# Performance work log

Hardware: AMD Instinct MI355X
Metric: run time of the kernel (lower is better)

The kernel has to match this reference:

```python
import jax, jax.numpy as jnp
import numpy as np

K = 20          # knn
EPS = 1e-5      # InstanceNorm2d eps
NEG_SLOPE = 0.2 # LeakyReLU slope


def setup_inputs() -> dict:
    key = jax.random.key(0)
    k1, k2 = jax.random.split(key)
    B, C, N = 4, 64, 4096
    out_dim, in_dim = 64, 2 * C
    batch = jax.random.normal(k1, (B, C, N), dtype=jnp.float32)
    # Conv2d(in_dim, out_dim, kernel_size=1, bias=False) weight, squeezed to [out,in]
    W = jax.random.normal(k2, (out_dim, in_dim), dtype=jnp.float32) * (1.0 / np.sqrt(in_dim))
    return {"batch": batch, "W": W}


def reference(batch, W):
    x = batch  # [B, C, N]
    # --- KNNGraph: pairwise squared distances + top-k nearest ---
    xx = jnp.sum(x * x, axis=1)                      # [B, N]
    inner = jnp.einsum('bcn,bcm->bnm', x, x)         # [B, N, N]
    neg_dist = -(xx[:, :, None] - 2.0 * inner + xx[:, None, :])  # [B, N, N]
    _, idx = jax.lax.top_k(neg_dist, K)              # [B, N, K] nearest neighbors
    # --- edge feature gather: concat(x_j - x_i, x_i) -> [B, 2C, N, K] ---
    nbr = jax.vmap(lambda xb, ib: xb[:, ib])(x, idx) # [B, C, N, K]
    center = x[:, :, :, None]                        # [B, C, N, 1]
    edge = jnp.concatenate([nbr - center, jnp.broadcast_to(center, nbr.shape)], axis=1)
    # --- 1x1 Conv2d (shared MLP, no bias) ---
    y = jnp.einsum('oc,bcnk->bonk', W, edge)         # [B, out, N, K]
    # --- InstanceNorm2d (no affine, biased var over spatial dims) ---
    mean = jnp.mean(y, axis=(2, 3), keepdims=True)
    var = jnp.var(y, axis=(2, 3), keepdims=True)
    y = (y - mean) * jax.lax.rsqrt(var + EPS)
    # --- LeakyReLU(0.2) ---
    y = jnp.where(y >= 0, y, NEG_SLOPE * y)
    # --- MaxPool over neighbor dim ---
    return jnp.max(y, axis=3)                        # [B, out, N]
```

## Files before the change

### kernel.cpp

```cpp
#include <hip/hip_runtime.h>
#include <hip/hip_bf16.h>
#include <cstdint>
#include <cstddef>

#define BB 4
#define NN 4096
#define NROW (BB*NN)
#define CAP3 128
#define ZSTAR 2.17f
#define SLACK 0.30

typedef float v2f   __attribute__((ext_vector_type(2)));
typedef float f32x16 __attribute__((ext_vector_type(16)));
typedef short s16x8 __attribute__((ext_vector_type(8)));
typedef _Float16 f16x8 __attribute__((ext_vector_type(8)));

__device__ __forceinline__ v2f pkfma(v2f a, v2f b, v2f c) {
  return __builtin_elementwise_fma(a, b, c);
}

__global__ __launch_bounds__(256) void k1_prep(
    const float* __restrict__ x, const float* __restrict__ W,
    float* __restrict__ xT, unsigned short* __restrict__ xh,
    float* __restrict__ xxf, double* __restrict__ xxd, float* __restrict__ Trow,
    float* __restrict__ uT, float* __restrict__ vT)
{
  __shared__ float xc[64][65];
  __shared__ float xr[64][68];
  __shared__ float w1[64][65];
  __shared__ float wd[64][65];
  int t = threadIdx.x;
  int b  = blockIdx.x >> 6;
  int n0 = (blockIdx.x & 63) * 64;

  for (int i = t; i < 4096; i += 256) {
    int o = i >> 6, c = i & 63;
    float a = W[o*128 + c];
    w1[o][c] = a;
    wd[o][c] = W[o*128 + 64 + c] - a;
  }
  for (int i = t; i < 4096; i += 256) {
    int c = i >> 6, n = i & 63;
    xc[c][n] = x[((size_t)b*64 + c)*4096 + n0 + n];
  }
  __syncthreads();

  for (int i = t; i < 4096; i += 256) {
    int n = i >> 6, c = i & 63;
    float v = xc[c][n];
    xr[n][c] = v;
    size_t pi = ((size_t)b*4096 + n0 + n)*64 + c;
    xT[pi] = v;
    xh[pi] = __builtin_bit_cast(unsigned short, (_Float16)v);
  }
  if (t < 64) {
    int n = t;
    float s0=0,s1=0,s2=0,s3=0; double sd=0.0;
    for (int c = 0; c < 64; c += 4) {
      float a0=xc[c][n],a1=xc[c+1][n],a2=xc[c+2][n],a3=xc[c+3][n];
      s0=fmaf(a0,a0,s0); s1=fmaf(a1,a1,s1); s2=fmaf(a2,a2,s2); s3=fmaf(a3,a3,s3);
      sd += (double)a0*a0 + (double)a1*a1 + (double)a2*a2 + (double)a3*a3;
    }
    float xxv = (s0+s1)+(s2+s3);
    size_t ri = (size_t)b*4096 + n0 + n;
    xxf[ri] = xxv;
    xxd[ri] = sd;
    Trow[ri] = fmaf(-ZSTAR, sqrtf(fmaf(4.0f, xxv, 128.0f)), 64.0f);
  }
  v2f w1r[32], wdr[32];
  int o = t & 63;
  #pragma unroll
  for (int j = 0; j < 32; ++j) {
    w1r[j].x = w1[o][2*j]; w1r[j].y = w1[o][2*j+1];
    wdr[j].x = wd[o][2*j]; wdr[j].y = wd[o][2*j+1];
  }
  __syncthreads();

  for (int i = t; i < 4096; i += 256) {
    int n = i >> 6;
    v2f au; au.x=0.f; au.y=0.f;
    v2f av; av.x=0.f; av.y=0.f;
    #pragma unroll
    for (int cb = 0; cb < 16; ++cb) {
      float4 xv = *(const float4*)&xr[n][cb*4];
      v2f p0; p0.x = xv.x; p0.y = xv.y;
      v2f p1; p1.x = xv.z; p1.y = xv.w;
      au = pkfma(w1r[2*cb],   p0, au);
      au = pkfma(w1r[2*cb+1], p1, au);
      av = pkfma(wdr[2*cb],   p0, av);
      av = pkfma(wdr[2*cb+1], p1, av);
    }
    size_t idx = ((size_t)b*4096 + n0 + n)*64 + o;
    uT[idx] = au.x + au.y;
    vT[idx] = av.x + av.y;
  }
}

__global__ __launch_bounds__(256) void k2_screen(
    const unsigned short* __restrict__ xh, const float* __restrict__ xxf,
    const float* __restrict__ Trow, unsigned* __restrict__ bitmap)
{
  int t  = threadIdx.x;
  int nb = blockIdx.x >> 4;
  int ms = blockIdx.x & 15;
  int row0 = nb * 256;
  int b = row0 >> 12;
  int mbase = ms * 256;
  const unsigned short* xhB = xh + ((size_t)b*4096)*64;

  int wv = t >> 6, lane = t & 63;
  int lr = lane & 31, oct = lane >> 5;

  s16x8 ah[2][4];
  #pragma unroll
  for (int nt = 0; nt < 2; ++nt)
    #pragma unroll
    for (int ks = 0; ks < 4; ++ks)
      ah[nt][ks] = *(const s16x8*)(xh +
        ((size_t)(row0 + wv*64 + nt*32 + lr))*64 + ks*16 + oct*8);

  float Ta[16], Tb[16];
  #pragma unroll
  for (int i = 0; i < 16; ++i) {
    int bi = (i & 3) + 8*(i >> 2);
    Ta[i] = Trow[row0 + wv*64 + bi + 4*oct];
    Tb[i] = Trow[row0 + wv*64 + 32 + bi + 4*oct];
  }

  unsigned mreg[8];
  #pragma unroll
  for (int mt = 0; mt < 8; ++mt) {
    int m0 = mbase + mt*32;
    float xxm = xxf[b*4096 + m0 + lr];
    s16x8 bh[4];
    #pragma unroll
    for (int ks = 0; ks < 4; ++ks)
      bh[ks] = *(const s16x8*)(xhB + (size_t)(m0 + lr)*64 + ks*16 + oct*8);

    f32x16 a0, a1;
    #pragma unroll
    for (int i = 0; i < 16; ++i) { a0[i] = 0.f; a1[i] = 0.f; }
    #pragma unroll
    for (int ks = 0; ks < 4; ++ks) {
      f16x8 AH0 = __builtin_bit_cast(f16x8, ah[0][ks]);
      f16x8 AH1 = __builtin_bit_cast(f16x8, ah[1][ks]);
      f16x8 BH  = __builtin_bit_cast(f16x8, bh[ks]);
      a0 = __builtin_amdgcn_mfma_f32_32x32x16_f16(AH0, BH, a0, 0, 0, 0);
      a1 = __builtin_amdgcn_mfma_f32_32x32x16_f16(AH1, BH, a1, 0, 0, 0);
    }

    unsigned mymask = 0u;
    #pragma unroll
    for (int i = 0; i < 16; ++i) {
      const int base_i = (i & 3) + 8*(i >> 2);
      {
        float w = fmaf(-2.0f, a0[i], xxm);
        unsigned long long mk = __ballot(w < Ta[i]);
        mymask = (lane == base_i)     ? (unsigned)mk         : mymask;
        mymask = (lane == base_i + 4) ? (unsigned)(mk >> 32) : mymask;
      }
      {
        float w = fmaf(-2.0f, a1[i], xxm);
        unsigned long long mk = __ballot(w < Tb[i]);
        mymask = (lane == 32 + base_i) ? (unsigned)mk         : mymask;
        mymask = (lane == 36 + base_i) ? (unsigned)(mk >> 32) : mymask;
      }
    }
    mreg[mt] = mymask;
  }

  size_t grow = (size_t)(row0 + wv*64 + lane);
  uint4 lo4; lo4.x = mreg[0]; lo4.y = mreg[1]; lo4.z = mreg[2]; lo4.w = mreg[3];
  uint4 hi4; hi4.x = mreg[4]; hi4.y = mreg[5]; hi4.z = mreg[6]; hi4.w = mreg[7];
  *(uint4*)&bitmap[grow*128 + ms*8]     = lo4;
  *(uint4*)&bitmap[grow*128 + ms*8 + 4] = hi4;
}

__global__ __launch_bounds__(256) void k3_select(
    const float* __restrict__ xT, const double* __restrict__ xxd,
    const float* __restrict__ Trow, const unsigned* __restrict__ bitmap,
    const float* __restrict__ uT, const float* __restrict__ vT,
    float* __restrict__ stage, double* __restrict__ pS1, double* __restrict__ pS2,
    unsigned* __restrict__ slowcnt, unsigned* __restrict__ slowlist)
{
  __shared__ unsigned short candm[4][CAP3];
  int wv = threadIdx.x >> 6, lane = threadIdx.x & 63;
  int row = blockIdx.x * 4 + wv;
  int b = row >> 12;

  double s1t = 0.0, s2t = 0.0;
  double xxn = xxd[row];

  uint2 wds = *(const uint2*)&bitmap[(size_t)row*128 + lane*2];
  int myc = __popc(wds.x) + __popc(wds.y);
  int inc = myc;
  #pragma unroll
  for (int d = 1; d < 64; d <<= 1) {
    int v = __shfl_up(inc, d);
    if (lane >= d) inc += v;
  }
  int total = __shfl(inc, 63);
  int off = inc - myc;
  bool slow = (total < 20) || (total > CAP3);

  if (!slow) {
    unsigned w = wds.x; int mb = lane*64;
    while (w) { int j = __ffs(w) - 1; w &= w - 1;
                candm[wv][off++] = (unsigned short)(mb + j); }
    w = wds.y; mb = lane*64 + 32;
    while (w) { int j = __ffs(w) - 1; w &= w - 1;
                candm[wv][off++] = (unsigned short)(mb + j); }
  }
  __builtin_amdgcn_wave_barrier();

  if (!slow) {
    const float* pn = xT + (size_t)row*64;
    int nr = (total + 63) >> 6;
    unsigned long long L = ~0ull;
    for (int r = 0; r < nr; ++r) {
      int ci = r*64 + lane;
      unsigned long long S = ~0ull;
      if (ci < total) {
        int m = (int)candm[wv][ci];
        const float* pm = xT + ((size_t)b*4096 + m)*64;
        double acc0 = 0.0, acc1 = 0.0;
        #pragma unroll
        for (int c5 = 0; c5 < 64; c5 += 4) {
          float4 A = *(const float4*)(pn + c5);
          float4 B = *(const float4*)(pm + c5);
          acc0 = fma((double)A.x, (double)B.x, acc0);
          acc1 = fma((double)A.y, (double)B.y, acc1);
          acc0 = fma((double)A.z, (double)B.z, acc0);
          acc1 = fma((double)A.w, (double)B.w, acc1);
        }
        double d = xxn + xxd[(size_t)b*4096 + m] - 2.0*(acc0 + acc1);
        d = fmax(d, 0.0);
        S = (((unsigned long long)__double_as_longlong(d)) & ~0xFFFull)
          | (unsigned long long)m;
      }
      #pragma unroll
      for (int kk = 2; kk <= 64; kk <<= 1) {
        #pragma unroll
        for (int j = kk >> 1; j > 0; j >>= 1) {
          unsigned long long o = __shfl_xor(S, j);
          bool up    = ((lane & kk) == 0);
          bool lower = ((lane & j) == 0);
          unsigned long long mn = (S < o) ? S : o;
          unsigned long long mx = (S < o) ? o : S;
          S = (lower == up) ? mn : mx;
        }
      }
      if (r == 0) {
        L = S;
      } else {
        unsigned long long Sr = __shfl(S, 63 - lane);
        unsigned long long lo = (L < Sr) ? L : Sr;
        #pragma unroll
        for (int j = 32; j > 0; j >>= 1) {
          unsigned long long o = __shfl_xor(lo, j);
          unsigned long long mn = (lo < o) ? lo : o;
          unsigned long long mx = (lo < o) ? o : lo;
          lo = ((lane & j) == 0) ? mn : mx;
        }
        L = lo;
      }
    }
    unsigned long long k19 = __shfl(L, 19);
    double d20 = __longlong_as_double((long long)(k19 & ~0xFFFull));
    float Tr = Trow[row];
    if (!(d20 - xxn < (double)Tr - SLACK)) {
      slow = true;
    } else {
      int mlow = (int)(L & 0xFFFull);
      const float* ub = uT + (size_t)b*4096*64;
      float mx = -3.4e38f, s1 = 0.f, s2 = 0.f;
      #pragma unroll
      for (int k = 0; k < 20; ++k) {
        int m = __shfl(mlow, k);
        float g = ub[(size_t)m*64 + lane];
        mx = fmaxf(mx, g); s1 += g; s2 = fmaf(g, g, s2);
      }
      size_t ro = (size_t)row*64 + lane;
      float v = vT[ro];
      stage[ro] = mx + v;
      double dv = (double)v;
      s1t = (double)s1 + 20.0*dv;
      s2t = (double)s2 + 2.0*dv*(double)s1 + 20.0*dv*dv;
    }
  }
  if (slow && lane == 0) {
    unsigned i = atomicAdd(slowcnt, 1u); slowlist[i] = row;
  }
  pS1[(size_t)row*64 + lane] = s1t;
  pS2[(size_t)row*64 + lane] = s2t;
}

__global__ __launch_bounds__(256) void k3b_slow(
    const float* __restrict__ xT, const double* __restrict__ xxd,
    const unsigned* __restrict__ slowcnt, const unsigned* __restrict__ slowlist,
    const float* __restrict__ uT, const float* __restrict__ vT,
    float* __restrict__ stage, double* __restrict__ k3bS1, double* __restrict__ k3bS2)
{
  __shared__ unsigned long long keyl[4096];
  __shared__ unsigned long long red[4];
  __shared__ unsigned t20[20];
  unsigned nslow = *slowcnt;
  int t = threadIdx.x;
  for (unsigned ii = blockIdx.x; ii < nslow; ii += gridDim.x) {
    int row = (int)slowlist[ii];
    int b = row >> 12, n = row & 4095;
    const float* pn = xT + ((size_t)b*4096 + n)*64;
    double xxn = xxd[(size_t)b*4096 + n];
    for (int m = t; m < 4096; m += 256) {
      const float* pm = xT + ((size_t)b*4096 + m)*64;
      double acc = 0.0;
      #pragma unroll 4
      for (int c = 0; c < 64; c += 4) {
        float4 a  = *(const float4*)(pn + c);
        float4 bf = *(const float4*)(pm + c);
        acc = fma((double)a.x, (double)bf.x, acc);
        acc = fma((double)a.y, (double)bf.y, acc);
        acc = fma((double)a.z, (double)bf.z, acc);
        acc = fma((double)a.w, (double)bf.w, acc);
      }
      double d = fmax(xxn + xxd[(size_t)b*4096 + m] - 2.0*acc, 0.0);
      keyl[m] = (((unsigned long long)__double_as_longlong(d)) & ~0xFFFull)
              | (unsigned long long)m;
    }
    __syncthreads();
    for (int k = 0; k < 20; ++k) {
      unsigned long long mn = ~0ull;
      #pragma unroll
      for (int s = 0; s < 16; ++s) {
        unsigned long long v = keyl[t + s*256];
        mn = (v < mn) ? v : mn;
      }
      for (int off = 32; off > 0; off >>= 1) {
        unsigned long long o = __shfl_down(mn, off);
        mn = (o < mn) ? o : mn;
      }
      if ((t & 63) == 0) red[t >> 6] = mn;
      __syncthreads();
      if (t == 0) {
        unsigned long long w0 = red[0];
        for (int q = 1; q < 4; ++q) w0 = (red[q] < w0) ? red[q] : w0;
        t20[k] = (unsigned)(w0 & 0xFFFull);
        keyl[w0 & 0xFFFull] = ~0ull;
      }
      __syncthreads();
    }
    if (t < 64) {
      const float* ub = uT + (size_t)b*4096*64;
      float mx = -3.4e38f, s1 = 0.f, s2 = 0.f;
      #pragma unroll
      for (int k = 0; k < 20; ++k) {
        unsigned m = t20[k];
        float g = ub[(size_t)m*64 + t];
        mx = fmaxf(mx, g); s1 += g; s2 = fmaf(g, g, s2);
      }
      size_t ro = ((size_t)b*4096 + n)*64 + t;
      float v = vT[ro];
      stage[ro] = mx + v;
      double dv = (double)v;
      __hip_atomic_fetch_add(&k3bS1[b*64 + t], (double)s1 + 20.0*dv,
                             __ATOMIC_RELAXED, __HIP_MEMORY_SCOPE_AGENT);
      __hip_atomic_fetch_add(&k3bS2[b*64 + t], (double)s2 + 2.0*dv*(double)s1 + 20.0*dv*dv,
                             __ATOMIC_RELAXED, __HIP_MEMORY_SCOPE_AGENT);
    }
    __syncthreads();
  }
}

__global__ __launch_bounds__(256) void k4a1_reduce(
    const double* __restrict__ pS1, const double* __restrict__ pS2,
    double* __restrict__ part1, double* __restrict__ part2)
{
  __shared__ double r1[4][64], r2[4][64];
  int blk = blockIdx.x;
  int t = threadIdx.x, wv = t >> 6, o = t & 63;
  size_t rbase = (size_t)blk*64 + wv*16;
  double s1 = 0.0, s2 = 0.0;
  for (int j = 0; j < 16; ++j) {
    s1 += pS1[(rbase + j)*64 + o];
    s2 += pS2[(rbase + j)*64 + o];
  }
  r1[wv][o] = s1; r2[wv][o] = s2;
  __syncthreads();
  if (wv == 0) {
    part1[(size_t)blk*64 + o] = r1[0][o]+r1[1][o]+r1[2][o]+r1[3][o];
    part2[(size_t)blk*64 + o] = r2[0][o]+r2[1][o]+r2[2][o]+r2[3][o];
  }
}

__global__ __launch_bounds__(256) void k4a2_params(
    const double* __restrict__ part1, const double* __restrict__ part2,
    const double* __restrict__ k3bS1, const double* __restrict__ k3bS2,
    float2* __restrict__ params)
{
  __shared__ double r1[4][64], r2[4][64];
  int b = blockIdx.x;
  int t = threadIdx.x, wv = t >> 6, o = t & 63;
  double s1 = 0.0, s2 = 0.0;
  for (int j = wv*16; j < wv*16 + 16; ++j) {
    s1 += part1[((size_t)b*64 + j)*64 + o];
    s2 += part2[((size_t)b*64 + j)*64 + o];
  }
  r1[wv][o] = s1; r2[wv][o] = s2;
  __syncthreads();
  if (wv == 0) {
    double S1 = k3bS1[b*64 + o] + r1[0][o]+r1[1][o]+r1[2][o]+r1[3][o];
    double S2 = k3bS2[b*64 + o] + r2[0][o]+r2[1][o]+r2[2][o]+r2[3][o];
    double inv = 1.0 / (4096.0 * 20.0);
    double mean = S1 * inv;
    double var  = S2 * inv - mean * mean;
    float2 pr; pr.x = (float)mean; pr.y = (float)rsqrt(var + 1e-5);
    params[b*64 + o] = pr;
  }
}

__global__ __launch_bounds__(256) void k4b_final(
    const float* __restrict__ stage, const float2* __restrict__ params,
    float* __restrict__ out)
{
  __shared__ float tile[64][65];
  int blk = blockIdx.x;
  int b = blk >> 6, n0 = (blk & 63) * 64;
  int t = threadIdx.x;
  int o = t & 63;
  float2 pr = params[b*64 + o];
  for (int i = t; i < 4096; i += 256) {
    int nn = i >> 6;
    float y = (stage[((size_t)b*4096 + n0 + nn)*64 + o] - pr.x) * pr.y;
    tile[nn][o] = (y >= 0.f) ? y : 0.2f * y;
  }
  __syncthreads();
  for (int i = t; i < 4096; i += 256) {
    int oo = i >> 6, nn = i & 63;
    out[((size_t)(b*64 + oo))*4096 + n0 + nn] = tile[nn][oo];
  }
}

extern "C" void kernel_launch(void* const* d_in, const int* in_sizes, int n_in,
                              void* d_out, int out_size, void* d_ws, size_t ws_size,
                              hipStream_t stream)
{
  (void)in_sizes; (void)n_in; (void)out_size; (void)ws_size;
  const float* x = (const float*)d_in[0];
  const float* W = (const float*)d_in[1];
  float* out = (float*)d_out;

  char* ws = (char*)d_ws;
  size_t off = 0;
  auto alloc = [&](size_t bytes) {
    char* p = ws + off;
    off = (off + bytes + 255) & ~(size_t)255;
    return p;
  };
  float*          uT       = (float*)         alloc((size_t)NROW*64*4);
  float*          vT       = (float*)         alloc((size_t)NROW*64*4);
  float*          xT       = (float*)         alloc((size_t)NROW*64*4);
  float*          stage    = (float*)         alloc((size_t)NROW*64*4);
  unsigned short* xh       = (unsigned short*)alloc((size_t)NROW*64*2);
  float*          xxf      = (float*)         alloc((size_t)NROW*4);
  double*         xxd      = (double*)        alloc((size_t)NROW*8);
  float*          Trow     = (float*)         alloc((size_t)NROW*4);
  double*         pS1      = (double*)        alloc((size_t)NROW*64*8);
  double*         pS2      = (double*)        alloc((size_t)NROW*64*8);
  double*         part1    = (double*)        alloc((size_t)256*64*8);
  double*         part2    = (double*)        alloc((size_t)256*64*8);
  unsigned*       bitmap   = (unsigned*)      alloc((size_t)NROW*128*4);
  float2*         params   = (float2*)        alloc(256*8);
  unsigned*       slowcnt  = (unsigned*)      alloc(256);
  double*         k3bS1    = (double*)        alloc(256*8);
  double*         k3bS2    = (double*)        alloc(256*8);
  unsigned*       slowlist = (unsigned*)      alloc((size_t)NROW*4);

  hipMemsetAsync(slowcnt, 0, 256 + 2048 + 2048, stream);

  k1_prep    <<<256,  256, 0, stream>>>(x, W, xT, xh, xxf, xxd, Trow, uT, vT);
  k2_screen  <<<1024, 256, 0, stream>>>(xh, xxf, Trow, bitmap);
  k3_select  <<<4096, 256, 0, stream>>>(xT, xxd, Trow, bitmap, uT, vT,
                                        stage, pS1, pS2, slowcnt, slowlist);
  k3b_slow   <<<256,  256, 0, stream>>>(xT, xxd, slowcnt, slowlist,
                                        uT, vT, stage, k3bS1, k3bS2);
  k4a1_reduce<<<256,  256, 0, stream>>>(pS1, pS2, part1, part2);
  k4a2_params<<<4,    256, 0, stream>>>(part1, part2, k3bS1, k3bS2, params);
  k4b_final  <<<256,  256, 0, stream>>>(stage, params, out);
}
```

Measured before the change: 149.6 us.

## Fold squared norm into MFMA via augmented fp16 rows and drop ballot masking

Each point's fp16 row is widened to 80 entries, with the squared norm (scaled by -0.5 through a constant in the other operand) placed in an extra K-slice. The distance threshold test then becomes a single compare of the MFMA output against a per-row constant. The screen kernel is also reorganized so each lane owns a query row and builds its bitmap words with bit ORs and one cross-half shuffle instead of 32 ballots per tile, and the tile shape changes to 128 rows by 512 columns. The fp16 norm loses precision and the extra K-slice adds MFMA work, so the candidate cap and slack are raised to absorb the extra candidates.

```diff
diff --git a/kernel.cpp b/kernel.cpp
--- a/kernel.cpp
+++ b/kernel.cpp
@@ -6,9 +6,9 @@
 #define BB 4
 #define NN 4096
 #define NROW (BB*NN)
-#define CAP3 128
+#define CAP3 192
 #define ZSTAR 2.17f
-#define SLACK 0.30
+#define SLACK 0.40
 
 typedef float v2f   __attribute__((ext_vector_type(2)));
 typedef float f32x16 __attribute__((ext_vector_type(16)));
@@ -21,8 +21,8 @@
 
 __global__ __launch_bounds__(256) void k1_prep(
     const float* __restrict__ x, const float* __restrict__ W,
-    float* __restrict__ xT, unsigned short* __restrict__ xh,
-    float* __restrict__ xxf, double* __restrict__ xxd, float* __restrict__ Trow,
+    float* __restrict__ xT, unsigned short* __restrict__ xh2,
+    double* __restrict__ xxd, float* __restrict__ Trow,
     float* __restrict__ uT, float* __restrict__ vT)
 {
   __shared__ float xc[64][65];
@@ -49,9 +49,9 @@
     int n = i >> 6, c = i & 63;
     float v = xc[c][n];
     xr[n][c] = v;
-    size_t pi = ((size_t)b*4096 + n0 + n)*64 + c;
-    xT[pi] = v;
-    xh[pi] = __builtin_bit_cast(unsigned short, (_Float16)v);
+    size_t pt = (size_t)b*4096 + n0 + n;
+    xT[pt*64 + c] = v;
+    xh2[pt*80 + c] = __builtin_bit_cast(unsigned short, (_Float16)v);
   }
   if (t < 64) {
     int n = t;
@@ -63,9 +63,12 @@
     }
     float xxv = (s0+s1)+(s2+s3);
     size_t ri = (size_t)b*4096 + n0 + n;
-    xxf[ri] = xxv;
     xxd[ri] = sd;
     Trow[ri] = fmaf(-ZSTAR, sqrtf(fmaf(4.0f, xxv, 128.0f)), 64.0f);
+    size_t xb2 = ri*80 + 64;
+    xh2[xb2] = __builtin_bit_cast(unsigned short, (_Float16)xxv);
+    #pragma unroll
+    for (int q = 1; q < 16; ++q) xh2[xb2 + q] = 0;
   }
   v2f w1r[32], wdr[32];
   int o = t & 63;
@@ -97,83 +100,71 @@
 }
 
 __global__ __launch_bounds__(256) void k2_screen(
-    const unsigned short* __restrict__ xh, const float* __restrict__ xxf,
-    const float* __restrict__ Trow, unsigned* __restrict__ bitmap)
+    const unsigned short* __restrict__ xh2, const float* __restrict__ Trow,
+    unsigned* __restrict__ bitmap)
 {
   int t  = threadIdx.x;
-  int nb = blockIdx.x >> 4;
-  int ms = blockIdx.x & 15;
-  int row0 = nb * 256;
+  int nblk = blockIdx.x >> 3;
+  int ms   = blockIdx.x & 7;
+  int row0 = nblk * 128;
   int b = row0 >> 12;
-  int mbase = ms * 256;
-  const unsigned short* xhB = xh + ((size_t)b*4096)*64;
-
   int wv = t >> 6, lane = t & 63;
   int lr = lane & 31, oct = lane >> 5;
-
-  s16x8 ah[2][4];
+  int n = row0 + wv*32 + lr;
+
+  s16x8 bn[5];
   #pragma unroll
-  for (int nt = 0; nt < 2; ++nt)
-    #pragma unroll
-    for (int ks = 0; ks < 4; ++ks)
-      ah[nt][ks] = *(const s16x8*)(xh +
-        ((size_t)(row0 + wv*64 + nt*32 + lr))*64 + ks*16 + oct*8);
-
-  float Ta[16], Tb[16];
-  #pragma unroll
-  for (int i = 0; i < 16; ++i) {
-    int bi = (i & 3) + 8*(i >> 2);
-    Ta[i] = Trow[row0 + wv*64 + bi + 4*oct];
-    Tb[i] = Trow[row0 + wv*64 + 32 + bi + 4*oct];
-  }
-
-  unsigned mreg[8];
-  #pragma unroll
+  for (int ks = 0; ks < 4; ++ks)
+    bn[ks] = *(const s16x8*)(xh2 + (size_t)n*80 + ks*16 + oct*8);
+  {
+    s16x8 z;
+    #pragma unroll
+    for (int q = 0; q < 8; ++q) z[q] = 0;
+    if (!oct) z[0] = (short)0xB800;
+    bn[4] = z;
+  }
+  float cn = -0.5f * Trow[n];
+
+  const unsigned short* xmB = xh2 + (size_t)b*4096*80;
+  int mbase = ms * 512;
+
   for (int mt = 0; mt < 8; ++mt) {
-    int m0 = mbase + mt*32;
-    float xxm = xxf[b*4096 + m0 + lr];
-    s16x8 bh[4];
-    #pragma unroll
-    for (int ks = 0; ks < 4; ++ks)
-      bh[ks] = *(const s16x8*)(xhB + (size_t)(m0 + lr)*64 + ks*16 + oct*8);
+    int m0 = mbase + mt*64;
+    s16x8 am0[5], am1[5];
+    #pragma unroll
+    for (int ks = 0; ks < 4; ++ks) {
+      am0[ks] = *(const s16x8*)(xmB + (size_t)(m0 + lr)*80      + ks*16 + oct*8);
+      am1[ks] = *(const s16x8*)(xmB + (size_t)(m0 + 32 + lr)*80 + ks*16 + oct*8);
+    }
+    am0[4] = *(const s16x8*)(xmB + (size_t)(m0 + lr)*80      + 64 + oct*8);
+    am1[4] = *(const s16x8*)(xmB + (size_t)(m0 + 32 + lr)*80 + 64 + oct*8);
 
     f32x16 a0, a1;
     #pragma unroll
     for (int i = 0; i < 16; ++i) { a0[i] = 0.f; a1[i] = 0.f; }
     #pragma unroll
-    for (int ks = 0; ks < 4; ++ks) {
-      f16x8 AH0 = __builtin_bit_cast(f16x8, ah[0][ks]);
-      f16x8 AH1 = __builtin_bit_cast(f16x8, ah[1][ks]);
-      f16x8 BH  = __builtin_bit_cast(f16x8, bh[ks]);
-      a0 = __builtin_amdgcn_mfma_f32_32x32x16_f16(AH0, BH, a0, 0, 0, 0);
-      a1 = __builtin_amdgcn_mfma_f32_32x32x16_f16(AH1, BH, a1, 0, 0, 0);
-    }
-
-    unsigned mymask = 0u;
+    for (int ks = 0; ks < 5; ++ks) {
+      f16x8 B = __builtin_bit_cast(f16x8, bn[ks]);
+      a0 = __builtin_amdgcn_mfma_f32_32x32x16_f16(
+             __builtin_bit_cast(f16x8, am0[ks]), B, a0, 0, 0, 0);
+      a1 = __builtin_amdgcn_mfma_f32_32x32x16_f16(
+             __builtin_bit_cast(f16x8, am1[ks]), B, a1, 0, 0, 0);
+    }
+
+    unsigned ua[4] = {0u,0u,0u,0u}, ub[4] = {0u,0u,0u,0u};
     #pragma unroll
     for (int i = 0; i < 16; ++i) {
-      const int base_i = (i & 3) + 8*(i >> 2);
-      {
-        float w = fmaf(-2.0f, a0[i], xxm);
-        unsigned long long mk = __ballot(w < Ta[i]);
-        mymask = (lane == base_i)     ? (unsigned)mk         : mymask;
-        mymask = (lane == base_i + 4) ? (unsigned)(mk >> 32) : mymask;
-      }
-      {
-        float w = fmaf(-2.0f, a1[i], xxm);
-        unsigned long long mk = __ballot(w < Tb[i]);
-        mymask = (lane == 32 + base_i) ? (unsigned)mk         : mymask;
-        mymask = (lane == 36 + base_i) ? (unsigned)(mk >> 32) : mymask;
-      }
-    }
-    mreg[mt] = mymask;
-  }
-
-  size_t grow = (size_t)(row0 + wv*64 + lane);
-  uint4 lo4; lo4.x = mreg[0]; lo4.y = mreg[1]; lo4.z = mreg[2]; lo4.w = mreg[3];
-  uint4 hi4; hi4.x = mreg[4]; hi4.y = mreg[5]; hi4.z = mreg[6]; hi4.w = mreg[7];
-  *(uint4*)&bitmap[grow*128 + ms*8]     = lo4;
-  *(uint4*)&bitmap[grow*128 + ms*8 + 4] = hi4;
+      int p = (i & 3) + 8*(i >> 2) + 4*oct;
+      unsigned bit = 1u << p;
+      ua[i & 3] = (a0[i] > cn) ? (ua[i & 3] | bit) : ua[i & 3];
+      ub[i & 3] = (a1[i] > cn) ? (ub[i & 3] | bit) : ub[i & 3];
+    }
+    unsigned u0 = (ua[0] | ua[1]) | (ua[2] | ua[3]);
+    unsigned u1 = (ub[0] | ub[1]) | (ub[2] | ub[3]);
+    unsigned w0 = u0 | (unsigned)__shfl_xor((int)u0, 32);
+    unsigned w1 = u1 | (unsigned)__shfl_xor((int)u1, 32);
+    bitmap[(size_t)n*128 + ms*16 + mt*2 + oct] = oct ? w1 : w0;
+  }
 }
 
 __global__ __launch_bounds__(256) void k3_select(
@@ -460,8 +451,7 @@
   float*          vT       = (float*)         alloc((size_t)NROW*64*4);
   float*          xT       = (float*)         alloc((size_t)NROW*64*4);
   float*          stage    = (float*)         alloc((size_t)NROW*64*4);
-  unsigned short* xh       = (unsigned short*)alloc((size_t)NROW*64*2);
-  float*          xxf      = (float*)         alloc((size_t)NROW*4);
+  unsigned short* xh2      = (unsigned short*)alloc((size_t)NROW*80*2);
   double*         xxd      = (double*)        alloc((size_t)NROW*8);
   float*          Trow     = (float*)         alloc((size_t)NROW*4);
   double*         pS1      = (double*)        alloc((size_t)NROW*64*8);
@@ -477,8 +467,8 @@
 
   hipMemsetAsync(slowcnt, 0, 256 + 2048 + 2048, stream);
 
-  k1_prep    <<<256,  256, 0, stream>>>(x, W, xT, xh, xxf, xxd, Trow, uT, vT);
-  k2_screen  <<<1024, 256, 0, stream>>>(xh, xxf, Trow, bitmap);
+  k1_prep    <<<256,  256, 0, stream>>>(x, W, xT, xh2, xxd, Trow, uT, vT);
+  k2_screen  <<<1024, 256, 0, stream>>>(xh2, Trow, bitmap);
   k3_select  <<<4096, 256, 0, stream>>>(xT, xxd, Trow, bitmap, uT, vT,
                                         stage, pS1, pS2, slowcnt, slowlist);
   k3b_slow   <<<256,  256, 0, stream>>>(xT, xxd, slowcnt, slowlist,
```

Result: no change. 148.4 us (-0.8%).
